# Kernel tuning notes

Hardware: AMD Instinct MI355X
Metric: run time of the kernel (lower is better)

## Reference

```python
import jax, jax.numpy as jnp
import numpy as np

B, T, N = 8, 100, 100000
MARGIN = 0.1
THRESHOLD = 0.5
BIG = 1.0e9


def setup_inputs() -> dict:
    key = jax.random.key(0)
    k0, k1, k2, k3, k4 = jax.random.split(key, 5)
    outputs = jax.random.normal(k0, (B, T, 3), dtype=jnp.float32)
    c2ws = jax.random.normal(k1, (B, 4, 4), dtype=jnp.float32)
    scene_scales = jax.random.uniform(k2, (B,), dtype=jnp.float32)
    means = jax.random.normal(k3, (N, 3), dtype=jnp.float32)
    scales = jax.random.uniform(k4, (N, 3), dtype=jnp.float32)
    return {"outputs": outputs, "c2ws": c2ws, "scene_scales": scene_scales,
            "means": means, "scales": scales}


def reference(outputs, c2ws, scene_scales, means, scales):
    # per-splat max radius (precomputed in torch __init__)
    maxsplatrad = jnp.max(scales, axis=1)                      # [N]
    # world transform: aff = R * scene_scale, trans = translation
    aff = c2ws[:, :3, :3] * scene_scales[:, None, None]        # [B,3,3]
    trans = c2ws[:, :3, 3]                                     # [B,3]
    # baddbmm(trans, outputs, aff.mT) == outputs @ aff^T + trans
    retrajs = jnp.einsum('btd,bed->bte', outputs, aff) + trans[:, None, :]  # [B,T,3]
    # axis-aligned bbox of each trajectory, expanded by threshold
    thres = THRESHOLD * scene_scales[0]
    uvals = jnp.max(retrajs, axis=1) + thres                   # [B,3]
    lvals = jnp.min(retrajs, axis=1) - thres                   # [B,3]
    # bbox filter: which splats fall inside each trajectory bbox
    inside = jnp.all((means[None, :, :] >= lvals[:, None, :]) &
                     (means[None, :, :] <= uvals[:, None, :]), axis=2)  # [B,N]
    # pairwise distances via ||a-b||^2 = |a|^2 + |b|^2 - 2 a.b (avoids [B,T,N,3])
    r2 = jnp.sum(retrajs * retrajs, axis=-1)                   # [B,T]
    m2 = jnp.sum(means * means, axis=-1)                       # [N]
    cross = jnp.einsum('btd,nd->btn', retrajs, means)          # [B,T,N]
    d2 = r2[:, :, None] + m2[None, None, :] - 2.0 * cross
    dist = jnp.sqrt(jnp.maximum(d2, 0.0))
    resdists = dist - maxsplatrad[None, None, :] - MARGIN      # [B,T,N]
    # scatter_reduce amin with include_self=False and 1e9 default ==
    # masked min over splats; pairs not inside bbox never scattered -> BIG
    masked = jnp.where(inside[:, None, :], resdists, BIG)
    collosses = jnp.min(masked, axis=2)                        # [B,T]
    return jnp.sum(jax.nn.relu(-collosses)) / (B * T)
```

## Files before the change

kernel.cpp:

```cpp
#include <hip/hip_runtime.h>

constexpr int   B_ = 8;
constexpr int   T_ = 100;
constexpr int   NPAIRS = B_ * T_;
constexpr int   N_ = 100000;
constexpr float MARGIN_ = 0.1f;
constexpr float THRESHOLD_ = 0.5f;
constexpr float BIG_ = 1000000000.0f;

constexpr int PER   = 98;
constexpr int NBLK  = 1024;
constexpr int NREC  = NBLK * PER;
constexpr int NSLOT = 1024;
constexpr int KCH   = 16;
constexpr int NRED  = NBLK / KCH;

constexpr size_t PACK_OFF   = 0;
constexpr size_t RES_OFF    = PACK_OFF + (size_t)NREC * 64;
constexpr size_t SLOT_OFF   = RES_OFF + (size_t)NBLK * NSLOT * 4;
constexpr size_t BOUNDS_OFF = SLOT_OFF + (size_t)NSLOT * 16;
constexpr size_t KEYS_OFF   = BOUNDS_OFF + 256;
constexpr size_t CNT_OFF    = KEYS_OFF + (size_t)NSLOT * 4;

__device__ __forceinline__ float fsqrt(float x) { return __builtin_amdgcn_sqrtf(x); }

__device__ __forceinline__ unsigned fkey(float f) {
    unsigned u = __float_as_uint(f);
    return (u & 0x80000000u) ? ~u : (u | 0x80000000u);
}

__global__ void k_prep(const float* __restrict__ outputs,
                       const float* __restrict__ c2ws,
                       const float* __restrict__ ss,
                       char* ws) {
    __shared__ float re_s[NPAIRS * 3];
    int tid = threadIdx.x;
    float* bounds = (float*)(ws + BOUNDS_OFF);

    ((unsigned*)(ws + KEYS_OFF))[tid] = fkey(BIG_);
    if (tid == 0) *(unsigned*)(ws + CNT_OFF) = 0;

    if (tid < NPAIRS) {
        int b = tid / T_;
        float s = ss[b];
        const float* o = outputs + tid * 3;
        float o0 = o[0], o1 = o[1], o2 = o[2];
        const float* c = c2ws + b * 16;
#pragma unroll
        for (int e = 0; e < 3; e++) {
            re_s[tid * 3 + e] =
                (o0 * c[e * 4 + 0] + o1 * c[e * 4 + 1] + o2 * c[e * 4 + 2]) * s + c[e * 4 + 3];
        }
    }
    __syncthreads();

    if (tid < 24) {
        int b = tid / 3, e = tid - b * 3;
        float mx = -3.4e38f, mn = 3.4e38f;
        for (int t = 0; t < T_; t++) {
            float v = re_s[(b * T_ + t) * 3 + e];
            mx = fmaxf(mx, v);
            mn = fminf(mn, v);
        }
        float thres = THRESHOLD_ * ss[0];
        bounds[b * 3 + e]      = mn - thres;
        bounds[24 + b * 3 + e] = mx + thres;
    }

    int bb = tid >> 7, r = tid & 127;
    float4 q = make_float4(0.f, 0.f, 0.f, 0.f);
    if (r < T_) {
        int p = bb * T_ + r;
        q = make_float4(re_s[p * 3 + 0], re_s[p * 3 + 1], re_s[p * 3 + 2], 1.f);
    }
    ((float4*)(ws + SLOT_OFF))[tid] = q;
}

__global__ __launch_bounds__(256) void k_pack(const float* __restrict__ means,
                                              const float* __restrict__ scales,
                                              char* ws) {
    int n = blockIdx.x * 256 + threadIdx.x;
    const float* bounds = (const float*)(ws + BOUNDS_OFF);
    float4* rec = (float4*)(ws + PACK_OFF + (size_t)n * 64);
    if (n < N_) {
        float mx = means[(size_t)n * 3 + 0];
        float my = means[(size_t)n * 3 + 1];
        float mz = means[(size_t)n * 3 + 2];
        float msr = fmaxf(fmaxf(scales[(size_t)n * 3 + 0], scales[(size_t)n * 3 + 1]),
                          scales[(size_t)n * 3 + 2]) + MARGIN_;
        float e[8];
#pragma unroll
        for (int b = 0; b < 8; b++) {
            bool in = (mx >= bounds[b * 3 + 0]) & (mx <= bounds[24 + b * 3 + 0]) &
                      (my >= bounds[b * 3 + 1]) & (my <= bounds[24 + b * 3 + 1]) &
                      (mz >= bounds[b * 3 + 2]) & (mz <= bounds[24 + b * 3 + 2]);
            e[b] = in ? msr : -BIG_;
        }
        rec[0] = make_float4(mx, my, mz, 0.f);
        rec[1] = make_float4(e[0], e[2], e[4], e[6]);
        rec[2] = make_float4(e[1], e[3], e[5], e[7]);
    } else {
        rec[0] = make_float4(0.f, 0.f, 0.f, 0.f);
        rec[1] = make_float4(-BIG_, -BIG_, -BIG_, -BIG_);
        rec[2] = make_float4(-BIG_, -BIG_, -BIG_, -BIG_);
    }
}

__global__ __launch_bounds__(256) void k_main(const char* __restrict__ wsc,
                                              char* __restrict__ ws) {
    int tid = threadIdx.x;
    const float4* sp = (const float4*)(wsc + SLOT_OFF);
    float4 q0 = sp[tid];
    float4 q1 = sp[tid + 256];
    float4 q2 = sp[tid + 512];
    float4 q3 = sp[tid + 768];

    int effoff = 16 + (((__builtin_amdgcn_readfirstlane(tid) >> 7) & 1) << 4);
    const char* rec = wsc + PACK_OFF + (size_t)blockIdx.x * PER * 64;

    float mn0 = BIG_, mn1 = BIG_, mn2 = BIG_, mn3 = BIG_;
#pragma unroll 2
    for (int i = 0; i < PER; i++) {
        float4 pos = *(const float4*)(rec);
        float4 ef  = *(const float4*)(rec + effoff);
        rec += 64;
        float dx, dy, dz, d2;
        dx = q0.x - pos.x; dy = q0.y - pos.y; dz = q0.z - pos.z;
        d2 = fmaf(dz, dz, fmaf(dy, dy, dx * dx));
        mn0 = fminf(mn0, fsqrt(d2) - ef.x);
        dx = q1.x - pos.x; dy = q1.y - pos.y; dz = q1.z - pos.z;
        d2 = fmaf(dz, dz, fmaf(dy, dy, dx * dx));
        mn1 = fminf(mn1, fsqrt(d2) - ef.y);
        dx = q2.x - pos.x; dy = q2.y - pos.y; dz = q2.z - pos.z;
        d2 = fmaf(dz, dz, fmaf(dy, dy, dx * dx));
        mn2 = fminf(mn2, fsqrt(d2) - ef.z);
        dx = q3.x - pos.x; dy = q3.y - pos.y; dz = q3.z - pos.z;
        d2 = fmaf(dz, dz, fmaf(dy, dy, dx * dx));
        mn3 = fminf(mn3, fsqrt(d2) - ef.w);
    }

    float* res = (float*)(ws + RES_OFF) + (size_t)blockIdx.x * NSLOT;
    res[tid]       = mn0;
    res[tid + 256] = mn1;
    res[tid + 512] = mn2;
    res[tid + 768] = mn3;
}

__global__ __launch_bounds__(256) void k_red(const char* __restrict__ wsc,
                                             char* __restrict__ ws,
                                             float* __restrict__ out) {
    __shared__ int   isLast;
    __shared__ float wsum[4];
    int tid = threadIdx.x;
    const float* res  = (const float*)(wsc + RES_OFF);
    unsigned*    keys = (unsigned*)(ws + KEYS_OFF);
    unsigned*    cnt  = (unsigned*)(ws + CNT_OFF);

    const float* row = res + (size_t)blockIdx.x * KCH * NSLOT;
    float mn0 = BIG_, mn1 = BIG_, mn2 = BIG_, mn3 = BIG_;
#pragma unroll
    for (int i = 0; i < KCH; i++) {
        mn0 = fminf(mn0, row[tid]);
        mn1 = fminf(mn1, row[tid + 256]);
        mn2 = fminf(mn2, row[tid + 512]);
        mn3 = fminf(mn3, row[tid + 768]);
        row += NSLOT;
    }
    atomicMin(&keys[tid],       fkey(mn0));
    atomicMin(&keys[tid + 256], fkey(mn1));
    atomicMin(&keys[tid + 512], fkey(mn2));
    atomicMin(&keys[tid + 768], fkey(mn3));

    __threadfence();
    if (tid == 0) isLast = (atomicAdd(cnt, 1u) == (unsigned)(NRED - 1));
    __syncthreads();
    if (isLast) {
        __threadfence();
        float acc = 0.f;
        for (int s = tid; s < NSLOT; s += 256) {
            if ((s & 127) < T_) {
                unsigned k = __hip_atomic_load(&keys[s], __ATOMIC_RELAXED, __HIP_MEMORY_SCOPE_AGENT);
                unsigned u = (k & 0x80000000u) ? (k ^ 0x80000000u) : ~k;
                acc += fmaxf(0.f, -__uint_as_float(u));
            }
        }
#pragma unroll
        for (int off = 32; off; off >>= 1) acc += __shfl_down(acc, off, 64);
        if ((tid & 63) == 0) wsum[tid >> 6] = acc;
        __syncthreads();
        if (tid == 0)
            out[0] = (wsum[0] + wsum[1] + wsum[2] + wsum[3]) * (1.0f / (float)NPAIRS);
    }
}

extern "C" void kernel_launch(void* const* d_in, const int* in_sizes, int n_in,
                              void* d_out, int out_size, void* d_ws, size_t ws_size,
                              hipStream_t stream) {
    const float* outputs = (const float*)d_in[0];
    const float* c2ws    = (const float*)d_in[1];
    const float* ss      = (const float*)d_in[2];
    const float* means   = (const float*)d_in[3];
    const float* scales  = (const float*)d_in[4];
    float* out = (float*)d_out;
    char*  ws  = (char*)d_ws;

    hipLaunchKernelGGL(k_prep, dim3(1), dim3(1024), 0, stream, outputs, c2ws, ss, ws);
    hipLaunchKernelGGL(k_pack, dim3(NREC / 256), dim3(256), 0, stream, means, scales, ws);
    hipLaunchKernelGGL(k_main, dim3(NBLK), dim3(256), 0, stream, (const char*)ws, ws);
    hipLaunchKernelGGL(k_red, dim3(NRED), dim3(256), 0, stream, (const char*)ws, ws, out);
}
```

Baseline: 109.6 us.

## Fuse splat packing into main kernel via shared-memory records

Removes the separate pack kernel. Each main block now loads its 98 splats, computes the per-batch bbox mask and effective radius, and stores the packed records in LDS. The distance loop then reads them from shared memory instead of from a global workspace. This saves one launch and the global write and read-back of the packed records, at the cost of a barrier and a serial prologue in each block where only 98 of 256 threads do work.

```diff
diff --git a/kernel.cpp b/kernel.cpp
--- a/kernel.cpp
+++ b/kernel.cpp
@@ -10,13 +10,11 @@
 
 constexpr int PER   = 98;
 constexpr int NBLK  = 1024;
-constexpr int NREC  = NBLK * PER;
 constexpr int NSLOT = 1024;
 constexpr int KCH   = 16;
 constexpr int NRED  = NBLK / KCH;
 
-constexpr size_t PACK_OFF   = 0;
-constexpr size_t RES_OFF    = PACK_OFF + (size_t)NREC * 64;
+constexpr size_t RES_OFF    = 0;
 constexpr size_t SLOT_OFF   = RES_OFF + (size_t)NBLK * NSLOT * 4;
 constexpr size_t BOUNDS_OFF = SLOT_OFF + (size_t)NSLOT * 16;
 constexpr size_t KEYS_OFF   = BOUNDS_OFF + 256;
@@ -76,54 +74,56 @@
     ((float4*)(ws + SLOT_OFF))[tid] = q;
 }
 
-__global__ __launch_bounds__(256) void k_pack(const float* __restrict__ means,
+__global__ __launch_bounds__(256) void k_main(const float* __restrict__ means,
                                               const float* __restrict__ scales,
-                                              char* ws) {
-    int n = blockIdx.x * 256 + threadIdx.x;
-    const float* bounds = (const float*)(ws + BOUNDS_OFF);
-    float4* rec = (float4*)(ws + PACK_OFF + (size_t)n * 64);
-    if (n < N_) {
-        float mx = means[(size_t)n * 3 + 0];
-        float my = means[(size_t)n * 3 + 1];
-        float mz = means[(size_t)n * 3 + 2];
-        float msr = fmaxf(fmaxf(scales[(size_t)n * 3 + 0], scales[(size_t)n * 3 + 1]),
-                          scales[(size_t)n * 3 + 2]) + MARGIN_;
-        float e[8];
-#pragma unroll
-        for (int b = 0; b < 8; b++) {
-            bool in = (mx >= bounds[b * 3 + 0]) & (mx <= bounds[24 + b * 3 + 0]) &
-                      (my >= bounds[b * 3 + 1]) & (my <= bounds[24 + b * 3 + 1]) &
-                      (mz >= bounds[b * 3 + 2]) & (mz <= bounds[24 + b * 3 + 2]);
-            e[b] = in ? msr : -BIG_;
-        }
-        rec[0] = make_float4(mx, my, mz, 0.f);
-        rec[1] = make_float4(e[0], e[2], e[4], e[6]);
-        rec[2] = make_float4(e[1], e[3], e[5], e[7]);
-    } else {
-        rec[0] = make_float4(0.f, 0.f, 0.f, 0.f);
-        rec[1] = make_float4(-BIG_, -BIG_, -BIG_, -BIG_);
-        rec[2] = make_float4(-BIG_, -BIG_, -BIG_, -BIG_);
-    }
-}
-
-__global__ __launch_bounds__(256) void k_main(const char* __restrict__ wsc,
+                                              const char* __restrict__ wsc,
                                               char* __restrict__ ws) {
+    __shared__ float4 rec_s[PER * 3];
     int tid = threadIdx.x;
-    const float4* sp = (const float4*)(wsc + SLOT_OFF);
+    const float4* sp     = (const float4*)(wsc + SLOT_OFF);
+    const float*  bounds = (const float*)(wsc + BOUNDS_OFF);
+
     float4 q0 = sp[tid];
     float4 q1 = sp[tid + 256];
     float4 q2 = sp[tid + 512];
     float4 q3 = sp[tid + 768];
 
-    int effoff = 16 + (((__builtin_amdgcn_readfirstlane(tid) >> 7) & 1) << 4);
-    const char* rec = wsc + PACK_OFF + (size_t)blockIdx.x * PER * 64;
+    if (tid < PER) {
+        int n = blockIdx.x * PER + tid;
+        float mx = 0.f, my = 0.f, mz = 0.f;
+        float e0, e1, e2, e3, e4, e5, e6, e7;
+        if (n < N_) {
+            mx = means[(size_t)n * 3 + 0];
+            my = means[(size_t)n * 3 + 1];
+            mz = means[(size_t)n * 3 + 2];
+            float msr = fmaxf(fmaxf(scales[(size_t)n * 3 + 0], scales[(size_t)n * 3 + 1]),
+                              scales[(size_t)n * 3 + 2]) + MARGIN_;
+            float e[8];
+#pragma unroll
+            for (int b = 0; b < 8; b++) {
+                bool in = (mx >= bounds[b * 3 + 0]) & (mx <= bounds[24 + b * 3 + 0]) &
+                          (my >= bounds[b * 3 + 1]) & (my <= bounds[24 + b * 3 + 1]) &
+                          (mz >= bounds[b * 3 + 2]) & (mz <= bounds[24 + b * 3 + 2]);
+                e[b] = in ? msr : -BIG_;
+            }
+            e0 = e[0]; e1 = e[1]; e2 = e[2]; e3 = e[3];
+            e4 = e[4]; e5 = e[5]; e6 = e[6]; e7 = e[7];
+        } else {
+            e0 = e1 = e2 = e3 = e4 = e5 = e6 = e7 = -BIG_;
+        }
+        rec_s[tid * 3 + 0] = make_float4(mx, my, mz, 0.f);
+        rec_s[tid * 3 + 1] = make_float4(e0, e2, e4, e6);
+        rec_s[tid * 3 + 2] = make_float4(e1, e3, e5, e7);
+    }
+    __syncthreads();
+
+    int effidx = 1 + ((__builtin_amdgcn_readfirstlane(tid) >> 7) & 1);
 
     float mn0 = BIG_, mn1 = BIG_, mn2 = BIG_, mn3 = BIG_;
 #pragma unroll 2
     for (int i = 0; i < PER; i++) {
-        float4 pos = *(const float4*)(rec);
-        float4 ef  = *(const float4*)(rec + effoff);
-        rec += 64;
+        float4 pos = rec_s[i * 3];
+        float4 ef  = rec_s[i * 3 + effidx];
         float dx, dy, dz, d2;
         dx = q0.x - pos.x; dy = q0.y - pos.y; dz = q0.z - pos.z;
         d2 = fmaf(dz, dz, fmaf(dy, dy, dx * dx));
@@ -205,7 +205,7 @@
     char*  ws  = (char*)d_ws;
 
     hipLaunchKernelGGL(k_prep, dim3(1), dim3(1024), 0, stream, outputs, c2ws, ss, ws);
-    hipLaunchKernelGGL(k_pack, dim3(NREC / 256), dim3(256), 0, stream, means, scales, ws);
-    hipLaunchKernelGGL(k_main, dim3(NBLK), dim3(256), 0, stream, (const char*)ws, ws);
+    hipLaunchKernelGGL(k_main, dim3(NBLK), dim3(256), 0, stream,
+                       means, scales, (const char*)ws, ws);
     hipLaunchKernelGGL(k_red, dim3(NRED), dim3(256), 0, stream, (const char*)ws, ws, out);
 }
```

Result: faster. 98.70 us (-9.9%).
